# Kernel optimization log

Measured on AMD Instinct MI355X. Metric: run time of the kernel, lower is better.

The kernel has to match this reference:

```python
import jax, jax.numpy as jnp
import numpy as np


def setup_inputs() -> dict:
    key = jax.random.key(0)
    ks = jax.random.split(key, 7)
    T, IN, H = 8192, 3000, 100
    s_ih = 1.0 / np.sqrt(H)
    return {
        "input_seq": jax.random.normal(ks[0], (T, IN), dtype=jnp.float32),
        "w_ih": jax.random.uniform(ks[1], (4 * H, IN), jnp.float32, -s_ih, s_ih),
        "w_hh": jax.random.uniform(ks[2], (4 * H, H), jnp.float32, -s_ih, s_ih),
        "b_ih": jax.random.uniform(ks[3], (4 * H,), jnp.float32, -s_ih, s_ih),
        "b_hh": jax.random.uniform(ks[4], (4 * H,), jnp.float32, -s_ih, s_ih),
        "w_lin": jax.random.uniform(ks[5], (1, H), jnp.float32, -s_ih, s_ih),
        "b_lin": jax.random.uniform(ks[6], (1,), jnp.float32, -s_ih, s_ih),
    }


def _lstm_scan(x_gates, w_hh, H):
    # x_gates: [T, 4H] precomputed input projections (incl. both biases)
    def step(carry, xg):
        h, c = carry
        g = xg + h @ w_hh.T  # [4H]
        i = jax.nn.sigmoid(g[:H])
        f = jax.nn.sigmoid(g[H:2 * H])
        gg = jnp.tanh(g[2 * H:3 * H])
        o = jax.nn.sigmoid(g[3 * H:])
        c = f * c + i * gg
        h = o * jnp.tanh(c)
        return (h, c), h

    h0 = jnp.zeros((H,), x_gates.dtype)
    c0 = jnp.zeros((H,), x_gates.dtype)
    _, hs = jax.lax.scan(step, (h0, c0), x_gates)
    return hs  # [T, H]


def reference(input_seq, w_ih, w_hh, b_ih, b_hh, w_lin, b_lin):
    H = w_hh.shape[1]
    # Fuse the per-timestep input GEMM into one big matmul (torch gate order i,f,g,o)
    x_gates = input_seq @ w_ih.T + b_ih + b_hh  # [T, 4H]
    hs = _lstm_scan(x_gates, w_hh, H)  # [T, H]
    preds = hs @ w_lin.T + b_lin  # [T, 1]
    return preds[-1]  # [1]
```

## Files before the change

kernel.cpp:

```cpp
#include <hip/hip_runtime.h>
#include <hip/hip_bf16.h>


#define GBM 128
#define GBN 128
#define GBK 16

typedef _Float16 h2_t __attribute__((ext_vector_type(2)));

__device__ __forceinline__ unsigned pk16(float a, float b) {
    h2_t p = {(_Float16)a, (_Float16)b};
    return __builtin_bit_cast(unsigned, p);
}

__global__ __launch_bounds__(256) void gates_gemm(
    const float* __restrict__ A,
    const float* __restrict__ W,
    const float* __restrict__ bih,
    const float* __restrict__ bhh,
    float* __restrict__ XG,
    int T, int IN, int FH)
{
    __shared__ __align__(16) unsigned As16[GBK / 2][GBM];
    __shared__ __align__(16) unsigned Bs16[GBK / 2][GBN];
    const int bm = blockIdx.x * GBM;
    const int bn = blockIdx.y * GBN;
    const int tid = (int)threadIdx.x;
    const int tx = tid & 15, ty = tid >> 4;
    const int H = FH >> 2;

    const int row0 = tid >> 2;
    const int row1 = (tid + 256) >> 2;
    const int kq0  = (tid & 3) << 2;
    const int kp0  = kq0 >> 1;
    const size_t aoff0 = (size_t)(bm + row0) * IN;
    const size_t aoff1 = (size_t)(bm + row1) * IN;
    const size_t boff0 = (size_t)(bn + row0) * IN;
    const size_t boff1 = (size_t)(bn + row1) * IN;
    const bool bok0 = (bn + row0) < FH;
    const bool bok1 = (bn + row1) < FH;

    float acc[8][8];
    #pragma unroll
    for (int i = 0; i < 8; ++i)
        #pragma unroll
        for (int j = 0; j < 8; ++j) acc[i][j] = 0.f;

    float4 z4 = make_float4(0.f, 0.f, 0.f, 0.f);
    float4 av0 = z4, av1 = z4, bv0 = z4, bv1 = z4;

    {
        int gk = kq0;
        if (gk < IN) {
            av0 = *(const float4*)&A[aoff0 + gk];
            av1 = *(const float4*)&A[aoff1 + gk];
            if (bok0) bv0 = *(const float4*)&W[boff0 + gk];
            if (bok1) bv1 = *(const float4*)&W[boff1 + gk];
        }
    }

    for (int k0 = 0; k0 < IN; k0 += GBK) {
        As16[kp0 + 0][row0] = pk16(av0.x, av0.y);
        As16[kp0 + 1][row0] = pk16(av0.z, av0.w);
        As16[kp0 + 0][row1] = pk16(av1.x, av1.y);
        As16[kp0 + 1][row1] = pk16(av1.z, av1.w);
        Bs16[kp0 + 0][row0] = pk16(bv0.x, bv0.y);
        Bs16[kp0 + 1][row0] = pk16(bv0.z, bv0.w);
        Bs16[kp0 + 0][row1] = pk16(bv1.x, bv1.y);
        Bs16[kp0 + 1][row1] = pk16(bv1.z, bv1.w);
        __syncthreads();

        {
            int gk = k0 + GBK + kq0;
            float4 na0 = z4, na1 = z4, nb0 = z4, nb1 = z4;
            if (gk < IN) {
                na0 = *(const float4*)&A[aoff0 + gk];
                na1 = *(const float4*)&A[aoff1 + gk];
                if (bok0) nb0 = *(const float4*)&W[boff0 + gk];
                if (bok1) nb1 = *(const float4*)&W[boff1 + gk];
            }
            av0 = na0; av1 = na1; bv0 = nb0; bv1 = nb1;
        }

        #pragma unroll
        for (int kk2 = 0; kk2 < GBK / 2; ++kk2) {
            uint4 ua0 = *(const uint4*)&As16[kk2][ty * 4];
            uint4 ua1 = *(const uint4*)&As16[kk2][64 + ty * 4];
            uint4 ub0 = *(const uint4*)&Bs16[kk2][tx * 4];
            uint4 ub1 = *(const uint4*)&Bs16[kk2][64 + tx * 4];
            h2_t ap[8] = {
                __builtin_bit_cast(h2_t, ua0.x), __builtin_bit_cast(h2_t, ua0.y),
                __builtin_bit_cast(h2_t, ua0.z), __builtin_bit_cast(h2_t, ua0.w),
                __builtin_bit_cast(h2_t, ua1.x), __builtin_bit_cast(h2_t, ua1.y),
                __builtin_bit_cast(h2_t, ua1.z), __builtin_bit_cast(h2_t, ua1.w)};
            h2_t bp[8] = {
                __builtin_bit_cast(h2_t, ub0.x), __builtin_bit_cast(h2_t, ub0.y),
                __builtin_bit_cast(h2_t, ub0.z), __builtin_bit_cast(h2_t, ub0.w),
                __builtin_bit_cast(h2_t, ub1.x), __builtin_bit_cast(h2_t, ub1.y),
                __builtin_bit_cast(h2_t, ub1.z), __builtin_bit_cast(h2_t, ub1.w)};
            #pragma unroll
            for (int i = 0; i < 8; ++i)
                #pragma unroll
                for (int j = 0; j < 8; ++j)
                    acc[i][j] = __builtin_amdgcn_fdot2(ap[i], bp[j], acc[i][j], false);
        }
        __syncthreads();
    }

    #pragma unroll
    for (int i = 0; i < 8; ++i) {
        int r = bm + ((i < 4) ? (ty * 4 + i) : (64 + ty * 4 + (i - 4)));
        #pragma unroll
        for (int j = 0; j < 8; ++j) {
            int cidx = bn + ((j < 4) ? (tx * 4 + j) : (64 + tx * 4 + (j - 4)));
            if (cidx < FH) {
                int pc = 4 * (cidx % H) + cidx / H;
                XG[(size_t)r * FH + pc] = acc[i][j] + bih[cidx] + bhh[cidx];
            }
        }
    }
}

__device__ __forceinline__ float pack_pair(const float* rp, int k) {
    float a = 0.f, b = 0.f;
    if (k < 100) { a = rp[k]; b = rp[k + 1]; }
    h2_t p = {(_Float16)a, (_Float16)b};
    return __builtin_bit_cast(float, p);
}

#define INITW(R, V) \
    asm volatile("v_mov_b32 v" #R ", %0" :: "v"(V) : "v" #R)

#define DD(A, W, Hr) "v_dot2_f32_f16 v" #A ", v" #W ", v" #Hr ", v" #A "\n\t"

#define VCLOB \
  "v96","v97","v98","v99","v100","v101","v102","v103","v104","v105","v106",\
  "v107","v108","v109","v110","v111","v112","v113","v114","v115","v116",\
  "v117","v118","v119","v120","v121","v122","v123","v124","v125","v126",\
  "v127","v128","v129","v130","v131","v132","v133","v134","v135","v136",\
  "v137","v138","v139","v140","v141","v142","v143","v144","v145","v146",\
  "v147","v148","v149","v150","v151","v152","v153","v154","v155","v156",\
  "v157","v158","v159","v160","v161","v162","v163","v164","v165","v166",\
  "v167","v168","v169","v170","v171","v172","v173","v174","v175","v176",\
  "v177","v178","v179","v180","v181","v182","v183","v184","v185","v186",\
  "v187","v188","v189","v190","v191","v192","v193","v194","v195","v196",\
  "v197","v198","v199","v200","v201","v202","v203","v204","v205","v206",\
  "v207","v208","v209","v210","v211","v212","v213","v214","v215","v216",\
  "v217","v218","v219","v220","v221","v222","v223","v224","v225","v226",\
  "v227","v228","v229","v230","v231","v232","v233","v234","v235","v236",\
  "v237","v238","v239","v240","v241","v242","v243","v244","v245","v246",\
  "v247","v248","v249","v250","v251","v252","v253","v254","v255"

#define BAR() asm volatile("s_waitcnt lgkmcnt(0)\n\ts_barrier" ::: "memory")

__global__ __launch_bounds__(256, 1) void lstm_scan_pinv5(
    const float* __restrict__ XGp,
    const float* __restrict__ Whh,
    const float* __restrict__ wlin,
    const float* __restrict__ blin,
    float* __restrict__ out, int T)
{
    __shared__ __align__(16) _Float16 hbuf[2][104];
    __shared__ float hfin[100];
    const int tid    = (int)threadIdx.x;
    const int parity = tid & 1;
    const int p      = tid >> 1;
    const int pc     = (p < 100) ? p : 99;
    const bool act   = (parity == 0) && (p < 100);
    const float kk   = 1.f + (float)parity;

    const float* r0p = Whh + (size_t)(pc + parity * 200) * 100;
    const float* r1p = Whh + (size_t)(pc + 100 + parity * 200) * 100;

#define LW(j, R0, R1) { INITW(R0, pack_pair(r0p, 2*(j))); \
                        INITW(R1, pack_pair(r1p, 2*(j))); }
    LW(0,152,204)  LW(1,153,205)  LW(2,154,206)  LW(3,155,207)
    LW(4,156,208)  LW(5,157,209)  LW(6,158,210)  LW(7,159,211)
    LW(8,160,212)  LW(9,161,213)  LW(10,162,214) LW(11,163,215)
    LW(12,164,216) LW(13,165,217) LW(14,166,218) LW(15,167,219)
    LW(16,168,220) LW(17,169,221) LW(18,170,222) LW(19,171,223)
    LW(20,172,224) LW(21,173,225) LW(22,174,226) LW(23,175,227)
    LW(24,176,228) LW(25,177,229) LW(26,178,230) LW(27,179,231)
    LW(28,180,232) LW(29,181,233) LW(30,182,234) LW(31,183,235)
    LW(32,184,236) LW(33,185,237) LW(34,186,238) LW(35,187,239)
    LW(36,188,240) LW(37,189,241) LW(38,190,242) LW(39,191,243)
    LW(40,192,244) LW(41,193,245) LW(42,194,246) LW(43,195,247)
    LW(48,200,252) LW(44,196,248) LW(45,197,249) LW(46,198,250)
    LW(47,199,251) LW(49,201,253) LW(50,202,254) LW(51,203,255)
#undef LW

    if (tid < 104) { hbuf[0][tid] = (_Float16)0.f; hbuf[1][tid] = (_Float16)0.f; }

    const unsigned hb_base = (unsigned)(uintptr_t)&hbuf[0][0];

    const int xoff = 4 * pc + 2 * parity;
#define XR(i) (*(const float2*)(XGp + (size_t)((i) < T ? (i) : (T - 1)) * 400 + xoff))

    float2 xa = XR(0), xb = XR(1), xc = XR(2), xd = XR(3);

    float c = 0.f, hlast = 0.f;
    int cur = 0;
    BAR();

#define MATVEC(G0, G1, HB, X0, X1) \
    asm volatile( \
        "v_mov_b32 v148, %[x0]\n\t" \
        "v_mov_b32 v149, %[x1]\n\t" \
        "v_mov_b32 v150, 0\n\t" \
        "v_mov_b32 v151, 0\n\t" \
        "ds_read_b128 v[96:99], %[hb]\n\t" \
        "ds_read_b128 v[100:103], %[hb] offset:16\n\t" \
        "ds_read_b128 v[104:107], %[hb] offset:32\n\t" \
        "ds_read_b128 v[108:111], %[hb] offset:48\n\t" \
        "ds_read_b128 v[112:115], %[hb] offset:64\n\t" \
        "ds_read_b128 v[116:119], %[hb] offset:80\n\t" \
        "ds_read_b128 v[120:123], %[hb] offset:96\n\t" \
        "ds_read_b128 v[124:127], %[hb] offset:112\n\t" \
        "ds_read_b128 v[128:131], %[hb] offset:128\n\t" \
        "ds_read_b128 v[132:135], %[hb] offset:144\n\t" \
        "ds_read_b128 v[136:139], %[hb] offset:160\n\t" \
        "ds_read_b128 v[140:143], %[hb] offset:176\n\t" \
        "ds_read_b128 v[144:147], %[hb] offset:192\n\t" \
        "s_waitcnt lgkmcnt(9)\n\t" \
        DD(148,152,96)  DD(149,204,96)  DD(150,153,97)  DD(151,205,97) \
        DD(148,154,98)  DD(149,206,98)  DD(150,155,99)  DD(151,207,99) \
        DD(148,156,100) DD(149,208,100) DD(150,157,101) DD(151,209,101) \
        DD(148,158,102) DD(149,210,102) DD(150,159,103) DD(151,211,103) \
        DD(148,160,104) DD(149,212,104) DD(150,161,105) DD(151,213,105) \
        DD(148,162,106) DD(149,214,106) DD(150,163,107) DD(151,215,107) \
        DD(148,164,108) DD(149,216,108) DD(150,165,109) DD(151,217,109) \
        DD(148,166,110) DD(149,218,110) DD(150,167,111) DD(151,219,111) \
        "s_waitcnt lgkmcnt(5)\n\t" \
        DD(148,168,112) DD(149,220,112) DD(150,169,113) DD(151,221,113) \
        DD(148,170,114) DD(149,222,114) DD(150,171,115) DD(151,223,115) \
        DD(148,172,116) DD(149,224,116) DD(150,173,117) DD(151,225,117) \
        DD(148,174,118) DD(149,226,118) DD(150,175,119) DD(151,227,119) \
        DD(148,176,120) DD(149,228,120) DD(150,177,121) DD(151,229,121) \
        DD(148,178,122) DD(149,230,122) DD(150,179,123) DD(151,231,123) \
        DD(148,180,124) DD(149,232,124) DD(150,181,125) DD(151,233,125) \
        DD(148,182,126) DD(149,234,126) DD(150,183,127) DD(151,235,127) \
        "s_waitcnt lgkmcnt(1)\n\t" \
        DD(148,184,128) DD(149,236,128) DD(150,185,129) DD(151,237,129) \
        DD(148,186,130) DD(149,238,130) DD(150,187,131) DD(151,239,131) \
        DD(148,188,132) DD(149,240,132) DD(150,189,133) DD(151,241,133) \
        DD(148,190,134) DD(149,242,134) DD(150,191,135) DD(151,243,135) \
        DD(148,192,136) DD(149,244,136) DD(150,193,137) DD(151,245,137) \
        DD(148,194,138) DD(149,246,138) DD(150,195,139) DD(151,247,139) \
        DD(148,196,140) DD(149,248,140) DD(150,197,141) DD(151,249,141) \
        DD(148,198,142) DD(149,250,142) DD(150,199,143) DD(151,251,143) \
        "s_waitcnt lgkmcnt(0)\n\t" \
        DD(148,200,144) DD(149,252,144) DD(150,201,145) DD(151,253,145) \
        DD(148,202,146) DD(149,254,146) DD(150,203,147) DD(151,255,147) \
        "v_add_f32 %[g0], v148, v150\n\t" \
        "v_add_f32 %[g1], v149, v151" \
        : [g0]"=v"(G0), [g1]"=v"(G1) \
        : [hb]"v"(HB), [x0]"v"(X0), [x1]"v"(X1) \
        : VCLOB, "memory")

#define SUBSTEP(XP, TNEXT) { \
    unsigned hb_ = hb_base + (unsigned)(cur * 208); \
    float g0, g1; \
    MATVEC(g0, g1, hb_, XP.x, XP.y); \
    XP = XR(TNEXT);    \
     \
    float e0  = __expf(kk * g0); \
    float t0v = 1.f - kk * __builtin_amdgcn_rcpf(e0 + 1.f); \
    float e1  = __expf(-g1); \
    float t1v = __builtin_amdgcn_rcpf(1.f + e1);    \
     \
    float rg_, ro_; \
    asm volatile("s_nop 3\n\t" \
                 "v_mov_b32 %0, %2 quad_perm:[1,0,3,2] row_mask:0xf bank_mask:0xf\n\t" \
                 "v_mov_b32 %1, %3 quad_perm:[1,0,3,2] row_mask:0xf bank_mask:0xf" \
                 : "=v"(rg_), "=v"(ro_) : "v"(t0v), "v"(t1v)); \
    c = fmaf(t1v, c, t0v * rg_);           \
    float e2 = __expf(2.f * c); \
    float th = 1.f - 2.f * __builtin_amdgcn_rcpf(e2 + 1.f); \
    float hv_ = ro_ * th;                  \
    if (act) { hlast = hv_; hbuf[cur ^ 1][p] = (_Float16)hv_; } \
    BAR(); \
    cur ^= 1; }

    for (int t = 0; t < T; t += 4) {
        SUBSTEP(xa, t + 4)
        SUBSTEP(xb, t + 5)
        SUBSTEP(xc, t + 6)
        SUBSTEP(xd, t + 7)
    }
#undef SUBSTEP
#undef XR

    if (act) hfin[p] = hlast * wlin[p];
    __syncthreads();
    if (tid == 0) {
        float s = blin[0];
        for (int k = 0; k < 100; ++k) s += hfin[k];
        out[0] = s;
    }
}

extern "C" void kernel_launch(void* const* d_in, const int* in_sizes, int n_in,
                              void* d_out, int out_size, void* d_ws, size_t ws_size,
                              hipStream_t stream) {
    const float* input = (const float*)d_in[0];
    const float* w_ih  = (const float*)d_in[1];
    const float* w_hh  = (const float*)d_in[2];
    const float* b_ih  = (const float*)d_in[3];
    const float* b_hh  = (const float*)d_in[4];
    const float* w_lin = (const float*)d_in[5];
    const float* b_lin = (const float*)d_in[6];
    float* out = (float*)d_out;

    const int FH = in_sizes[3];
    const int IN = in_sizes[1] / FH;
    const int T  = in_sizes[0] / IN;

    float* xg = (float*)d_ws;

    dim3 grid((T + GBM - 1) / GBM, (FH + GBN - 1) / GBN);
    gates_gemm<<<grid, 256, 0, stream>>>(input, w_ih, b_ih, b_hh, xg, T, IN, FH);
    lstm_scan_pinv5<<<1, 256, 0, stream>>>(xg, w_hh, w_lin, b_lin, out, T);
}
```

Baseline: 3.839 ms.

## Fuse input GEMM with LSTM scan using flag-synchronized producer blocks

```diff
diff --git a/kernel.cpp b/kernel.cpp
--- a/kernel.cpp
+++ b/kernel.cpp
@@ -14,12 +14,9 @@
 }
 
 __global__ __launch_bounds__(256) void gates_gemm(
-    const float* __restrict__ A,
-    const float* __restrict__ W,
-    const float* __restrict__ bih,
-    const float* __restrict__ bhh,
-    float* __restrict__ XG,
-    int T, int IN, int FH)
+    const float* __restrict__ A, const float* __restrict__ W,
+    const float* __restrict__ bih, const float* __restrict__ bhh,
+    float* __restrict__ XG, int T, int IN, int FH)
 {
     __shared__ __align__(16) unsigned As16[GBK / 2][GBM];
     __shared__ __align__(16) unsigned Bs16[GBK / 2][GBN];
@@ -48,7 +45,6 @@
 
     float4 z4 = make_float4(0.f, 0.f, 0.f, 0.f);
     float4 av0 = z4, av1 = z4, bv0 = z4, bv1 = z4;
-
     {
         int gk = kq0;
         if (gk < IN) {
@@ -58,7 +54,6 @@
             if (bok1) bv1 = *(const float4*)&W[boff1 + gk];
         }
     }
-
     for (int k0 = 0; k0 < IN; k0 += GBK) {
         As16[kp0 + 0][row0] = pk16(av0.x, av0.y);
         As16[kp0 + 1][row0] = pk16(av0.z, av0.w);
@@ -69,7 +64,6 @@
         Bs16[kp0 + 0][row1] = pk16(bv1.x, bv1.y);
         Bs16[kp0 + 1][row1] = pk16(bv1.z, bv1.w);
         __syncthreads();
-
         {
             int gk = k0 + GBK + kq0;
             float4 na0 = z4, na1 = z4, nb0 = z4, nb1 = z4;
@@ -81,7 +75,6 @@
             }
             av0 = na0; av1 = na1; bv0 = nb0; bv1 = nb1;
         }
-
         #pragma unroll
         for (int kk2 = 0; kk2 < GBK / 2; ++kk2) {
             uint4 ua0 = *(const uint4*)&As16[kk2][ty * 4];
@@ -106,7 +99,6 @@
         }
         __syncthreads();
     }
-
     #pragma unroll
     for (int i = 0; i < 8; ++i) {
         int r = bm + ((i < 4) ? (ty * 4 + i) : (64 + ty * 4 + (i - 4)));
@@ -119,6 +111,11 @@
             }
         }
     }
+}
+
+__global__ __launch_bounds__(64) void zero_flags(int* f, int n) {
+    int i = (int)threadIdx.x;
+    if (i < n) f[i] = 0;
 }
 
 __device__ __forceinline__ float pack_pair(const float* rp, int k) {
@@ -153,16 +150,120 @@
 
 #define BAR() asm volatile("s_waitcnt lgkmcnt(0)\n\ts_barrier" ::: "memory")
 
-__global__ __launch_bounds__(256, 1) void lstm_scan_pinv5(
-    const float* __restrict__ XGp,
+__global__ __launch_bounds__(256, 1) void lstm_fused(
+    const float* __restrict__ A,
+    const float* __restrict__ Wih,
+    const float* __restrict__ bih,
+    const float* __restrict__ bhh,
+    float* __restrict__ XGp,
     const float* __restrict__ Whh,
     const float* __restrict__ wlin,
     const float* __restrict__ blin,
-    float* __restrict__ out, int T)
+    float* __restrict__ out,
+    int* flags,
+    int T, int IN, int FH)
 {
     __shared__ __align__(16) _Float16 hbuf[2][104];
     __shared__ float hfin[100];
-    const int tid    = (int)threadIdx.x;
+    __shared__ __align__(16) unsigned As16[8][32];
+    __shared__ __align__(16) unsigned Bs16[8][128];
+
+    const int tid = (int)threadIdx.x;
+
+    if (blockIdx.x != 0) {
+        if (!flags) return;
+        const int H = FH >> 2;
+        const int ntile = (T >> 5) * 4;
+        const int tx = tid & 31, ty = tid >> 5;
+        const int sr   = tid >> 2;
+        const int skq  = (tid & 3) << 2;
+        const int skp  = skq >> 1;
+        const bool aok = tid < 128;
+
+        for (int tau = (int)blockIdx.x - 1; tau < ntile; tau += 255) {
+            const int rb = tau >> 2, cb = tau & 3;
+            const int bm = rb * 32, bn = cb * 128;
+            const size_t aoff  = (size_t)(bm + sr) * IN;
+            const size_t boff0 = (size_t)(bn + sr) * IN;
+            const size_t boff1 = (size_t)(bn + 64 + sr) * IN;
+            const bool bok0 = (bn + sr) < FH;
+            const bool bok1 = (bn + 64 + sr) < FH;
+
+            float acc[4][4];
+            #pragma unroll
+            for (int i = 0; i < 4; ++i)
+                #pragma unroll
+                for (int j = 0; j < 4; ++j) acc[i][j] = 0.f;
+
+            float4 z4 = make_float4(0.f, 0.f, 0.f, 0.f);
+            float4 av = z4, bv0 = z4, bv1 = z4;
+            {
+                int gk = skq;
+                if (gk < IN) {
+                    if (aok)  av  = *(const float4*)&A[aoff + gk];
+                    if (bok0) bv0 = *(const float4*)&Wih[boff0 + gk];
+                    if (bok1) bv1 = *(const float4*)&Wih[boff1 + gk];
+                }
+            }
+            for (int k0 = 0; k0 < IN; k0 += 16) {
+                if (aok) {
+                    As16[skp + 0][sr] = pk16(av.x, av.y);
+                    As16[skp + 1][sr] = pk16(av.z, av.w);
+                }
+                Bs16[skp + 0][sr]      = pk16(bv0.x, bv0.y);
+                Bs16[skp + 1][sr]      = pk16(bv0.z, bv0.w);
+                Bs16[skp + 0][64 + sr] = pk16(bv1.x, bv1.y);
+                Bs16[skp + 1][64 + sr] = pk16(bv1.z, bv1.w);
+                __syncthreads();
+                {
+                    int gk = k0 + 16 + skq;
+                    float4 na = z4, nb0 = z4, nb1 = z4;
+                    if (gk < IN) {
+                        if (aok)  na  = *(const float4*)&A[aoff + gk];
+                        if (bok0) nb0 = *(const float4*)&Wih[boff0 + gk];
+                        if (bok1) nb1 = *(const float4*)&Wih[boff1 + gk];
+                    }
+                    av = na; bv0 = nb0; bv1 = nb1;
+                }
+                #pragma unroll
+                for (int kk2 = 0; kk2 < 8; ++kk2) {
+                    uint4 ua = *(const uint4*)&As16[kk2][ty * 4];
+                    uint4 ub = *(const uint4*)&Bs16[kk2][tx * 4];
+                    h2_t ap[4] = {
+                        __builtin_bit_cast(h2_t, ua.x), __builtin_bit_cast(h2_t, ua.y),
+                        __builtin_bit_cast(h2_t, ua.z), __builtin_bit_cast(h2_t, ua.w)};
+                    h2_t bp[4] = {
+                        __builtin_bit_cast(h2_t, ub.x), __builtin_bit_cast(h2_t, ub.y),
+                        __builtin_bit_cast(h2_t, ub.z), __builtin_bit_cast(h2_t, ub.w)};
+                    #pragma unroll
+                    for (int i = 0; i < 4; ++i)
+                        #pragma unroll
+                        for (int j = 0; j < 4; ++j)
+                            acc[i][j] = __builtin_amdgcn_fdot2(ap[i], bp[j], acc[i][j], false);
+                }
+                __syncthreads();
+            }
+            #pragma unroll
+            for (int i = 0; i < 4; ++i) {
+                int r = bm + ty * 4 + i;
+                #pragma unroll
+                for (int j = 0; j < 4; ++j) {
+                    int cidx = bn + tx * 4 + j;
+                    if (cidx < FH) {
+                        int pc = 4 * (cidx % H) + cidx / H;
+                        XGp[(size_t)r * FH + pc] = acc[i][j] + bih[cidx] + bhh[cidx];
+                    }
+                }
+            }
+            __threadfence();
+            __syncthreads();
+            if (tid == 0)
+                __hip_atomic_fetch_add(flags + (rb >> 2), 1,
+                                       __ATOMIC_RELEASE, __HIP_MEMORY_SCOPE_AGENT);
+        }
+        return;
+    }
+
     const int parity = tid & 1;
     const int p      = tid >> 1;
     const int pc     = (p < 100) ? p : 99;
@@ -192,10 +293,21 @@
     if (tid < 104) { hbuf[0][tid] = (_Float16)0.f; hbuf[1][tid] = (_Float16)0.f; }
 
     const unsigned hb_base = (unsigned)(uintptr_t)&hbuf[0][0];
-
     const int xoff = 4 * pc + 2 * parity;
+
+#define WAITCH(c) { \
+    if (tid == 0) { \
+        while (__hip_atomic_load(flags + (c), __ATOMIC_ACQUIRE, \
+                                 __HIP_MEMORY_SCOPE_AGENT) < 16) {} \
+    } \
+    __syncthreads(); \
+    int f_ = __hip_atomic_load(flags + (c), __ATOMIC_ACQUIRE, \
+                               __HIP_MEMORY_SCOPE_AGENT); \
+    asm volatile("" :: "v"(f_)); }
+
 #define XR(i) (*(const float2*)(XGp + (size_t)((i) < T ? (i) : (T - 1)) * 400 + xoff))
 
+    if (flags) WAITCH(0);
     float2 xa = XR(0), xb = XR(1), xc = XR(2), xd = XR(3);
 
     float c = 0.f, hlast = 0.f;
@@ -261,27 +373,26 @@
     unsigned hb_ = hb_base + (unsigned)(cur * 208); \
     float g0, g1; \
     MATVEC(g0, g1, hb_, XP.x, XP.y); \
-    XP = XR(TNEXT);    \
-     \
+    XP = XR(TNEXT); \
     float e0  = __expf(kk * g0); \
     float t0v = 1.f - kk * __builtin_amdgcn_rcpf(e0 + 1.f); \
     float e1  = __expf(-g1); \
-    float t1v = __builtin_amdgcn_rcpf(1.f + e1);    \
-     \
+    float t1v = __builtin_amdgcn_rcpf(1.f + e1); \
     float rg_, ro_; \
     asm volatile("s_nop 3\n\t" \
                  "v_mov_b32 %0, %2 quad_perm:[1,0,3,2] row_mask:0xf bank_mask:0xf\n\t" \
                  "v_mov_b32 %1, %3 quad_perm:[1,0,3,2] row_mask:0xf bank_mask:0xf" \
                  : "=v"(rg_), "=v"(ro_) : "v"(t0v), "v"(t1v)); \
-    c = fmaf(t1v, c, t0v * rg_);           \
+    c = fmaf(t1v, c, t0v * rg_); \
     float e2 = __expf(2.f * c); \
     float th = 1.f - 2.f * __builtin_amdgcn_rcpf(e2 + 1.f); \
-    float hv_ = ro_ * th;                  \
+    float hv_ = ro_ * th; \
     if (act) { hlast = hv_; hbuf[cur ^ 1][p] = (_Float16)hv_; } \
     BAR(); \
     cur ^= 1; }
 
     for (int t = 0; t < T; t += 4) {
+        if (flags && (t & 127) == 120 && (t + 8) < T) WAITCH((t + 8) >> 7);
         SUBSTEP(xa, t + 4)
         SUBSTEP(xb, t + 5)
         SUBSTEP(xc, t + 6)
@@ -289,6 +400,7 @@
     }
 #undef SUBSTEP
 #undef XR
+#undef WAITCH
 
     if (act) hfin[p] = hlast * wlin[p];
     __syncthreads();
@@ -316,8 +428,21 @@
     const int T  = in_sizes[0] / IN;
 
     float* xg = (float*)d_ws;
-
-    dim3 grid((T + GBM - 1) / GBM, (FH + GBN - 1) / GBN);
-    gates_gemm<<<grid, 256, 0, stream>>>(input, w_ih, b_ih, b_hh, xg, T, IN, FH);
-    lstm_scan_pinv5<<<1, 256, 0, stream>>>(xg, w_hh, w_lin, b_lin, out, T);
-}
+    const size_t xg_bytes = (size_t)T * FH * 4;
+    const int nchunks = (T + 127) >> 7;
+
+    const bool overlap = (ws_size >= xg_bytes + 256) && (T % 128 == 0);
+    if (overlap) {
+        int* flags = (int*)((char*)d_ws + xg_bytes);
+        zero_flags<<<1, 64, 0, stream>>>(flags, nchunks);
+        lstm_fused<<<256, 256, 0, stream>>>(input, w_ih, b_ih, b_hh, xg,
+                                            w_hh, w_lin, b_lin, out, flags,
+                                            T, IN, FH);
+    } else {
+        dim3 grid((T + GBM - 1) / GBM, (FH + GBN - 1) / GBN);
+        gates_gemm<<<grid, 256, 0, stream>>>(input, w_ih, b_ih, b_hh, xg, T, IN, FH);
+        lstm_fused<<<1, 256, 0, stream>>>(input, w_ih, b_ih, b_hh, xg,
+                                          w_hh, w_lin, b_lin, out, nullptr,
+                                          T, IN, FH);
+    }
+}
```

New measurement: 3.815 ms. Within noise of the previous version (-0.6%).
